# Performance work log

Measured on AMD Instinct MI355X. Metric: run time of the kernel, lower is better.

## Reference

```python
import jax, jax.numpy as jnp
import numpy as np

B, N, C, H = 8, 1024, 1024, 16
D = C // H
DFF = 4 * C
EPS = 1e-6


def _ln(x):
    mu = jnp.mean(x, axis=-1, keepdims=True)
    var = jnp.mean(jnp.square(x - mu), axis=-1, keepdims=True)
    return (x - mu) / jnp.sqrt(var + EPS)


def _modulate(x, shift, scale):
    return x * (1 + scale) + shift


def setup_inputs() -> dict:
    key = jax.random.key(0)
    ks = jax.random.split(key, 12)
    s = 0.02
    inp = {
        "x": jax.random.normal(ks[0], (B, N, C), jnp.float32),
        "c": jax.random.normal(ks[1], (B, 1, C), jnp.float32),
        "causal_mask": jnp.tril(jnp.ones((N, N), jnp.int32))[None, None],  # [1,1,N,N]
        "qkv_w": jax.random.normal(ks[2], (3 * C, C), jnp.float32) * s,
        "qkv_b": jnp.zeros((3 * C,), jnp.float32),
        "proj_w": jax.random.normal(ks[3], (C, C), jnp.float32) * s,
        "proj_b": jnp.zeros((C,), jnp.float32),
        "fc1_w": jax.random.normal(ks[4], (DFF, C), jnp.float32) * s,
        "fc1_b": jnp.zeros((DFF,), jnp.float32),
        "fc2_w": jax.random.normal(ks[5], (C, DFF), jnp.float32) * s,
        "fc2_b": jnp.zeros((C,), jnp.float32),
        "ada_w": jax.random.normal(ks[6], (6 * C, C), jnp.float32) * s,
        "ada_b": jnp.zeros((6 * C,), jnp.float32),
    }
    return inp


def reference(x, c, causal_mask, qkv_w, qkv_b, proj_w, proj_b,
              fc1_w, fc1_b, fc2_w, fc2_b, ada_w, ada_b):
    # adaLN modulation: SiLU -> Linear(C -> 6C) -> chunk 6
    mod = jax.nn.silu(c) @ ada_w.T + ada_b  # [B,1,6C]
    (shift_msa, scale_msa, gate_msa,
     shift_mlp, scale_mlp, gate_mlp) = jnp.split(mod, 6, axis=-1)

    # --- causal attention ---
    y = _modulate(_ln(x), shift_msa, scale_msa)  # [B,N,C]
    qkv = y @ qkv_w.T + qkv_b                    # [B,N,3C]
    qkv = qkv.reshape(B, N, 3, H, D).transpose(2, 0, 3, 1, 4)  # [3,B,H,N,D]
    q, k, v = qkv[0], qkv[1], qkv[2]
    scale = D ** -0.5
    attn = jnp.einsum('bhnd,bhmd->bhnm', q, k) * scale  # [B,H,N,N]
    attn = jnp.where(causal_mask == 0, -jnp.inf, attn)
    attn = jax.nn.softmax(attn, axis=-1)
    o = jnp.einsum('bhnm,bhmd->bhnd', attn, v)
    o = o.transpose(0, 2, 1, 3).reshape(B, N, C)
    o = o @ proj_w.T + proj_b
    x = x + gate_msa * o

    # --- MLP ---
    z = _modulate(_ln(x), shift_mlp, scale_mlp)
    h = jax.nn.gelu(z @ fc1_w.T + fc1_b, approximate=True)
    m = h @ fc2_w.T + fc2_b
    x = x + gate_mlp * m
    return x
```

## Files before the change

kernel.cpp:

```cpp
#include <hip/hip_runtime.h>
#include <math.h>
#include <stdint.h>
#include <stddef.h>

namespace {

constexpr int kB = 8, kN = 1024, kC = 1024, kH = 16, kD = 64, kDFF = 4096;
constexpr int kM = kB * kN;
constexpr int k6C = 6 * kC;
constexpr float kQKScale = 0.18033688011112042f;
constexpr float kM8 = 8.0f;

typedef _Float16 half8 __attribute__((ext_vector_type(8)));
typedef _Float16 half4v __attribute__((ext_vector_type(4)));
typedef float f32x4 __attribute__((ext_vector_type(4)));
typedef int v4i __attribute__((ext_vector_type(4)));
typedef signed char i8;

__device__ inline void ld_lds16(const void* g, void* l) {
  __builtin_amdgcn_global_load_lds(
      (const __attribute__((address_space(1))) void*)g,
      (__attribute__((address_space(3))) void*)l, 16, 0, 0);
}

__device__ inline int xcd_swizzle(int flat, int nwg) {
  return (flat & 7) * (nwg >> 3) + (flat >> 3);
}

__device__ inline unsigned pack4_i8(float y0, float y1, float y2, float y3, float inv) {
  int q0 = (int)rintf(y0 * inv), q1 = (int)rintf(y1 * inv);
  int q2 = (int)rintf(y2 * inv), q3 = (int)rintf(y3 * inv);
  q0 = min(max(q0, -127), 127); q1 = min(max(q1, -127), 127);
  q2 = min(max(q2, -127), 127); q3 = min(max(q3, -127), 127);
  return (unsigned)(q0 & 0xFF) | ((unsigned)(q1 & 0xFF) << 8) |
         ((unsigned)(q2 & 0xFF) << 16) | ((unsigned)(q3 & 0xFF) << 24);
}

__global__ void cvt_f32_f16(const float* __restrict__ src, _Float16* __restrict__ dst) {
  size_t i = (size_t)blockIdx.x * 256 + threadIdx.x;
  float4 f = ((const float4*)src)[i];
  half4v h;
  h[0] = (_Float16)f.x; h[1] = (_Float16)f.y; h[2] = (_Float16)f.z; h[3] = (_Float16)f.w;
  ((half4v*)dst)[i] = h;
}

__global__ __launch_bounds__(256) void quant_w_kernel(
    const float* __restrict__ src, i8* __restrict__ dst, float* __restrict__ wscale) {
  int n = blockIdx.x, tid = threadIdx.x;
  const float* row = src + (size_t)n * kC;
  float4 f = ((const float4*)row)[tid];
  float m = fmaxf(fmaxf(fabsf(f.x), fabsf(f.y)), fmaxf(fabsf(f.z), fabsf(f.w)));
#pragma unroll
  for (int msk = 32; msk; msk >>= 1) m = fmaxf(m, __shfl_xor(m, msk));
  __shared__ float red[4];
  int w = tid >> 6, lane = tid & 63;
  if (lane == 0) red[w] = m;
  __syncthreads();
  m = fmaxf(fmaxf(red[0], red[1]), fmaxf(red[2], red[3]));
  m = fmaxf(m, 1e-12f);
  float inv = 127.f / m;
  ((unsigned*)(dst + (size_t)n * kC))[tid] = pack4_i8(f.x, f.y, f.z, f.w, inv);
  if (tid == 0) wscale[n] = m * (1.f / 127.f);
}

__global__ __launch_bounds__(256) void mod_kernel(
    const float* __restrict__ c, const float* __restrict__ ada_w,
    const float* __restrict__ ada_b, float* __restrict__ mod) {
  __shared__ float sc[kC];
  int b  = blockIdx.x / (k6C / 4);
  int j0 = (blockIdx.x % (k6C / 4)) * 4;
  int tid = threadIdx.x;
  for (int i = tid; i < kC; i += 256) {
    float v = c[b * kC + i];
    sc[i] = v / (1.f + expf(-v));
  }
  __syncthreads();
  int w = tid >> 6, lane = tid & 63;
  int j = j0 + w;
  const float* wr = ada_w + (size_t)j * kC;
  float acc = 0.f;
#pragma unroll
  for (int kk = 0; kk < kC / 64; ++kk) {
    int k = kk * 64 + lane;
    acc += sc[k] * wr[k];
  }
#pragma unroll
  for (int m = 32; m; m >>= 1) acc += __shfl_xor(acc, m);
  if (lane == 0) mod[b * k6C + j] = acc + ada_b[j];
}

template <typename T>
__global__ __launch_bounds__(256) void ln_mod_q_kernel(
    const T* __restrict__ x, const float* __restrict__ mod,
    i8* __restrict__ out, float* __restrict__ ascale,
    int shift_off, int scale_off) {
  int row = blockIdx.x;
  int b = row >> 10;
  const T* xr = x + (size_t)row * kC;
  int tid = threadIdx.x;
  int cc0 = tid * 4;
  float v[4];
  float s = 0.f, s2 = 0.f;
#pragma unroll
  for (int i = 0; i < 4; ++i) {
    v[i] = (float)xr[cc0 + i];
    s += v[i];
    s2 += v[i] * v[i];
  }
#pragma unroll
  for (int m = 32; m; m >>= 1) { s += __shfl_xor(s, m); s2 += __shfl_xor(s2, m); }
  __shared__ float red[8];
  __shared__ float redm[4];
  int w = tid >> 6, lane = tid & 63;
  if (lane == 0) { red[w] = s; red[4 + w] = s2; }
  __syncthreads();
  s  = red[0] + red[1] + red[2] + red[3];
  s2 = red[4] + red[5] + red[6] + red[7];
  float mu   = s * (1.f / kC);
  float var  = s2 * (1.f / kC) - mu * mu;
  float rstd = rsqrtf(var + 1e-6f);
  const float* mb = mod + (size_t)b * k6C;
  float y[4];
  float m = 0.f;
#pragma unroll
  for (int i = 0; i < 4; ++i) {
    y[i] = (v[i] - mu) * rstd * (1.f + mb[scale_off + cc0 + i]) + mb[shift_off + cc0 + i];
    m = fmaxf(m, fabsf(y[i]));
  }
#pragma unroll
  for (int msk = 32; msk; msk >>= 1) m = fmaxf(m, __shfl_xor(m, msk));
  if (lane == 0) redm[w] = m;
  __syncthreads();
  m = fmaxf(fmaxf(redm[0], redm[1]), fmaxf(redm[2], redm[3]));
  m = fmaxf(m, 1e-12f);
  float inv = 127.f / m;
  ((unsigned*)(out + (size_t)row * kC))[tid] = pack4_i8(y[0], y[1], y[2], y[3], inv);
  if (tid == 0) ascale[row] = m * (1.f / 127.f);
}

template <int EPI>
__global__ __launch_bounds__(256, 4) void gemm_i8_kernel(
    const i8* __restrict__ A, const i8* __restrict__ W,
    const float* __restrict__ ascale, const float* __restrict__ wscale,
    const float* __restrict__ bias, _Float16* __restrict__ outp,
    int M, int Nn, int K) {
  __shared__ __align__(16) i8 S[2 * 2 * 128 * 64];
  int tid = threadIdx.x;
  int nwg = (int)(gridDim.x * gridDim.y);
  int swz = xcd_swizzle((int)(blockIdx.y * gridDim.x + blockIdx.x), nwg);
  int bn = swz % (int)gridDim.x, bm = swz / (int)gridDim.x;
  int lane = tid & 63, w = tid >> 6;
  int l15 = lane & 15, quad = lane >> 4;
  int wr = (w >> 1) * 64, wc = (w & 1) * 64;

  v4i acc[4][4];
#pragma unroll
  for (int i = 0; i < 4; ++i)
#pragma unroll
    for (int j = 0; j < 4; ++j) acc[i][j] = (v4i){0, 0, 0, 0};

  const i8* Ag = A + (size_t)bm * 128 * K;
  const i8* Wg = W + (size_t)bn * 128 * K;
  int rg = lane >> 2;
  int gsl = lane & 3;

  auto stage = [&](int buf, int kt) {
    i8* As = S + buf * (2 * 128 * 64);
    i8* Bs = As + 128 * 64;
#pragma unroll
    for (int s = 0; s < 2; ++s) {
      int row = w * 32 + s * 16 + rg;
      int gc = (gsl ^ ((row >> 1) & 3)) * 16;
      ld_lds16(&Ag[(size_t)row * K + kt + gc], &As[(w * 32 + s * 16) * 64]);
      ld_lds16(&Wg[(size_t)row * K + kt + gc], &Bs[(w * 32 + s * 16) * 64]);
    }
  };

  int nk = K >> 6;
  stage(0, 0);
  stage(1, 64);

  int cread = (quad ^ ((l15 >> 1) & 3)) * 16;
  for (int t = 0; t < nk; ++t) {
    if (t + 1 < nk) {
      asm volatile("s_waitcnt vmcnt(4)" ::: "memory");
    } else {
      asm volatile("s_waitcnt vmcnt(0)" ::: "memory");
    }
    __builtin_amdgcn_s_barrier();
    __builtin_amdgcn_sched_barrier(0);
    const i8* As = S + (t & 1) * (2 * 128 * 64);
    const i8* Bs = As + 128 * 64;
    v4i af[4], bf[4];
#pragma unroll
    for (int i = 0; i < 4; ++i)
      af[i] = *(const v4i*)&As[(wr + i * 16 + l15) * 64 + cread];
#pragma unroll
    for (int j = 0; j < 4; ++j)
      bf[j] = *(const v4i*)&Bs[(wc + j * 16 + l15) * 64 + cread];
#pragma unroll
    for (int i = 0; i < 4; ++i)
#pragma unroll
      for (int j = 0; j < 4; ++j)
        acc[i][j] = __builtin_amdgcn_mfma_i32_16x16x64_i8(af[i], bf[j], acc[i][j], 0, 0, 0);
    asm volatile("s_waitcnt lgkmcnt(0)" ::: "memory");
    __builtin_amdgcn_sched_barrier(0);
    __builtin_amdgcn_s_barrier();
    __builtin_amdgcn_sched_barrier(0);
    if (t + 2 < nk) stage(t & 1, (t + 2) << 6);
  }

  _Float16* Cs = (_Float16*)S;
  int row0 = wr + quad * 4;
  int col0 = wc + l15;
#pragma unroll
  for (int i = 0; i < 4; ++i) {
#pragma unroll
    for (int j = 0; j < 4; ++j) {
      int colL = col0 + j * 16;
      int n = bn * 128 + colL;
      float ws = wscale[n];
      float bv = bias[n];
#pragma unroll
      for (int r = 0; r < 4; ++r) {
        int rowL = row0 + i * 16 + r;
        float as = ascale[bm * 128 + rowL];
        float v = (float)acc[i][j][r] * (as * ws) + bv;
        if constexpr (EPI == 0) {
          if (n < kC) v *= kQKScale;
        } else {
          float u = v + 0.044715f * v * v * v;
          float t = exp2f(-2.302208f * u);
          v = v * __builtin_amdgcn_rcpf(1.f + t);
        }
        Cs[rowL * 128 + (((colL >> 3) ^ (rowL & 7)) << 3) + (colL & 7)] = (_Float16)v;
      }
    }
  }
  __syncthreads();
#pragma unroll
  for (int p = 0; p < 8; ++p) {
    int r = (tid >> 4) + p * 16;
    int cc = tid & 15;
    half8 hv = *(const half8*)&Cs[r * 128 + ((cc ^ (r & 7)) << 3)];
    size_t gm = (size_t)(bm * 128 + r);
    int coff = bn * 128 + cc * 8;
    *(half8*)&outp[gm * Nn + coff] = hv;
  }
}

template <int EPI>
__global__ __launch_bounds__(256) void gemm_f16_kernel(
    const _Float16* __restrict__ A, const _Float16* __restrict__ W,
    const float* __restrict__ bias, void* __restrict__ outp,
    const void* __restrict__ resid, const float* __restrict__ mod,
    int M, int Nn, int K, int gate_off) {
  __shared__ __align__(16) _Float16 S[2 * 2 * 128 * 64];
  int tid = threadIdx.x;
  int nwg = (int)(gridDim.x * gridDim.y);
  int swz = xcd_swizzle((int)(blockIdx.y * gridDim.x + blockIdx.x), nwg);
  int bn = swz % (int)gridDim.x, bm = swz / (int)gridDim.x;
  int lane = tid & 63, w = tid >> 6;
  int l15 = lane & 15, quad = lane >> 4;
  int wr = (w >> 1) * 64, wc = (w & 1) * 64;

  f32x4 acc[4][4];
#pragma unroll
  for (int i = 0; i < 4; ++i)
#pragma unroll
    for (int j = 0; j < 4; ++j) acc[i][j] = (f32x4){0.f, 0.f, 0.f, 0.f};

  const _Float16* Ag = A + (size_t)bm * 128 * K;
  const _Float16* Wg = W + (size_t)bn * 128 * K;
  int r8 = lane >> 3;
  int jc = ((lane & 7) ^ r8) * 8;

  auto stage = [&](int buf, int kt) {
    _Float16* Asn = S + buf * (2 * 128 * 64);
    _Float16* Bsn = Asn + 128 * 64;
#pragma unroll
    for (int u = 0; u < 4; ++u) {
      int row = w * 32 + u * 8 + r8;
      ld_lds16(&Ag[(size_t)row * K + kt + jc], &Asn[(w * 32 + u * 8) * 64]);
      ld_lds16(&Wg[(size_t)row * K + kt + jc], &Bsn[(w * 32 + u * 8) * 64]);
    }
  };

  int nk = K / 64;
  stage(0, 0);
  stage(1, 64);

  for (int t = 0; t < nk; ++t) {
    if (t + 1 < nk) {
      asm volatile("s_waitcnt vmcnt(8)" ::: "memory");
    } else {
      asm volatile("s_waitcnt vmcnt(0)" ::: "memory");
    }
    __builtin_amdgcn_s_barrier();
    __builtin_amdgcn_sched_barrier(0);
    const _Float16* As = S + (t & 1) * (2 * 128 * 64);
    const _Float16* Bs = As + 128 * 64;
    half8 af[2][4], bf[2][4];
#pragma unroll
    for (int kk = 0; kk < 2; ++kk) {
#pragma unroll
      for (int i = 0; i < 4; ++i)
        af[kk][i] = *(const half8*)&As[(wr + i * 16 + l15) * 64 +
                                       (((kk * 4 + quad) ^ (l15 & 7)) * 8)];
#pragma unroll
      for (int j = 0; j < 4; ++j)
        bf[kk][j] = *(const half8*)&Bs[(wc + j * 16 + l15) * 64 +
                                       (((kk * 4 + quad) ^ (l15 & 7)) * 8)];
    }
#pragma unroll
    for (int kk = 0; kk < 2; ++kk)
#pragma unroll
      for (int i = 0; i < 4; ++i)
#pragma unroll
        for (int j = 0; j < 4; ++j)
          acc[i][j] = __builtin_amdgcn_mfma_f32_16x16x32_f16(af[kk][i], bf[kk][j],
                                                             acc[i][j], 0, 0, 0);
    asm volatile("s_waitcnt lgkmcnt(0)" ::: "memory");
    __builtin_amdgcn_sched_barrier(0);
    __builtin_amdgcn_s_barrier();
    __builtin_amdgcn_sched_barrier(0);
    if (t + 2 < nk) stage(t & 1, (t + 2) * 64);
  }

  _Float16* Cs = S;
  int row0 = wr + quad * 4;
  int col0 = wc + l15;
#pragma unroll
  for (int i = 0; i < 4; ++i) {
#pragma unroll
    for (int j = 0; j < 4; ++j) {
      int colL = col0 + j * 16;
      int n = bn * 128 + colL;
      float bv = bias[n];
#pragma unroll
      for (int r = 0; r < 4; ++r) {
        int rowL = row0 + i * 16 + r;
        float v = acc[i][j][r] + bv;
        Cs[rowL * 128 + (((colL >> 3) ^ (rowL & 7)) << 3) + (colL & 7)] = (_Float16)v;
      }
    }
  }
  __syncthreads();
  int b6 = (bm >> 3) * k6C + gate_off + bn * 128;
#pragma unroll
  for (int p = 0; p < 8; ++p) {
    int r = (tid >> 4) + p * 16;
    int cc = tid & 15;
    half8 hv = *(const half8*)&Cs[r * 128 + ((cc ^ (r & 7)) << 3)];
    size_t gm = (size_t)(bm * 128 + r);
    int coff = bn * 128 + cc * 8;
    if constexpr (EPI == 2) {
      const float* rp = &((const float*)resid)[gm * kC + coff];
      const float* gp = &mod[b6 + cc * 8];
      half8 ov;
#pragma unroll
      for (int e = 0; e < 8; ++e) ov[e] = (_Float16)(rp[e] + gp[e] * (float)hv[e]);
      *(half8*)&((_Float16*)outp)[gm * kC + coff] = ov;
    } else {
      const _Float16* rp = &((const _Float16*)resid)[gm * kC + coff];
      const float* gp = &mod[b6 + cc * 8];
      half8 rv = *(const half8*)rp;
      float ov[8];
#pragma unroll
      for (int e = 0; e < 8; ++e) ov[e] = (float)rv[e] + gp[e] * (float)hv[e];
      *(float4*)&((float*)outp)[gm * kC + coff] = *(float4*)&ov[0];
      *(float4*)&((float*)outp)[gm * kC + coff + 4] = *(float4*)&ov[4];
    }
  }
}

__global__ __launch_bounds__(256) void vtrans_kernel(
    const _Float16* __restrict__ qkv, _Float16* __restrict__ vT) {
  int nt = blockIdx.x, h = blockIdx.y, b = blockIdx.z;
  __shared__ _Float16 Ts[64 * 72];
  int tid = threadIdx.x;
  const _Float16* src = qkv + ((size_t)(b * kN + nt * 64)) * (3 * kC) + 2 * kC + h * 64;
#pragma unroll
  for (int u = 0; u < 2; ++u) {
    int idx = tid + u * 256;
    int r = idx >> 3, c8 = (idx & 7) * 8;
    *(uint4*)&Ts[r * 72 + c8] = *(const uint4*)&src[(size_t)r * (3 * kC) + c8];
  }
  __syncthreads();
  _Float16* dst = vT + (((size_t)(b * kH + h)) * 64) * kN + nt * 64;
#pragma unroll
  for (int u = 0; u < 2; ++u) {
    int idx = tid + u * 256;
    int d = idx >> 3, n8 = (idx & 7) * 8;
    half8 v;
#pragma unroll
    for (int e = 0; e < 8; ++e) v[e] = Ts[(n8 + e) * 72 + d];
    *(half8*)&dst[(size_t)d * kN + n8] = v;
  }
}

__global__ __launch_bounds__(256, 3) void attn_kernel(
    const _Float16* __restrict__ qkv, const _Float16* __restrict__ vT,
    _Float16* __restrict__ o) {
  int nwg = (int)(gridDim.x * gridDim.y * gridDim.z);
  int flat = (int)((blockIdx.z * gridDim.y + blockIdx.y) * gridDim.x + blockIdx.x);
  int swz = xcd_swizzle(flat, nwg);
  int qt = swz % (int)gridDim.x;
  int tmp = swz / (int)gridDim.x;
  int h = tmp % (int)gridDim.y, b = tmp / (int)gridDim.y;
  __shared__ __align__(16) _Float16 S[2 * 8192 + 128 * 72];
  _Float16* Ps = S + 16384;
  int tid = threadIdx.x, lane = tid & 63, w = tid >> 6;
  int l15 = lane & 15, quad = lane >> 4;
  int wq = w * 32;
  int r8 = lane >> 3;
  int jc = ((lane & 7) ^ r8) * 8;

  const _Float16* Qg = qkv + ((size_t)(b * kN + qt * 128)) * (3 * kC) + h * kD;
  const _Float16* Kg = qkv + ((size_t)(b * kN)) * (3 * kC) + kC + h * kD;
  const _Float16* Vg = vT + ((size_t)(b * kH + h) * kD) * kN;

  auto stage_kv = [&](_Float16* dstK, int j) {
#pragma unroll
    for (int u = 0; u < 2; ++u) {
      int row = w * 16 + u * 8 + r8;
      ld_lds16(&Kg[(size_t)(j * 64 + row) * (3 * kC) + jc], &dstK[(w * 16 + u * 8) * 64]);
      ld_lds16(&Vg[(size_t)row * kN + j * 64 + jc], &dstK[4096 + (w * 16 + u * 8) * 64]);
    }
  };

#pragma unroll
  for (int u = 0; u < 4; ++u)
    ld_lds16(&Qg[(size_t)(w * 32 + u * 8 + r8) * (3 * kC) + jc],
             &S[(w * 32 + u * 8) * 64]);
  stage_kv(S + 8192, 0);
  asm volatile("s_waitcnt vmcnt(4)" ::: "memory");
  __builtin_amdgcn_s_barrier();

  half8 aq[2][2];
#pragma unroll
  for (int i = 0; i < 2; ++i)
#pragma unroll
    for (int kk = 0; kk < 2; ++kk)
      aq[i][kk] = *(const half8*)&S[(wq + i * 16 + l15) * 64 +
                                    (((kk * 4 + quad) ^ (l15 & 7)) * 8)];
  asm volatile("s_waitcnt lgkmcnt(0)" ::: "memory");
  __builtin_amdgcn_sched_barrier(0);
  __builtin_amdgcn_s_barrier();
  stage_kv(S, 1);

  f32x4 o_acc[2][4];
  f32x4 lsum[2];
#pragma unroll
  for (int i = 0; i < 2; ++i) {
    lsum[i] = (f32x4){0.f, 0.f, 0.f, 0.f};
#pragma unroll
    for (int dt = 0; dt < 4; ++dt) o_acc[i][dt] = (f32x4){0.f, 0.f, 0.f, 0.f};
  }
  half8 ones;
#pragma unroll
  for (int e = 0; e < 8; ++e) ones[e] = (_Float16)1.f;

  int jmax = 2 * qt + 2;
  for (int j = 0; j < jmax; ++j) {
    if (j + 1 < jmax) {
      asm volatile("s_waitcnt vmcnt(4)" ::: "memory");
    } else {
      asm volatile("s_waitcnt vmcnt(0)" ::: "memory");
    }
    __builtin_amdgcn_s_barrier();
    __builtin_amdgcn_sched_barrier(0);
    const _Float16* Ks = (j & 1) ? S : S + 8192;
    const _Float16* Vs = Ks + 4096;
    bool need_mask = (j >= 2 * qt);

    f32x4 s[2][4];
#pragma unroll
    for (int ct = 0; ct < 4; ++ct) {
      half8 b0 = *(const half8*)&Ks[(ct * 16 + l15) * 64 + ((quad ^ (l15 & 7)) * 8)];
      half8 b1 = *(const half8*)&Ks[(ct * 16 + l15) * 64 + (((4 + quad) ^ (l15 & 7)) * 8)];
#pragma unroll
      for (int i = 0; i < 2; ++i) {
        f32x4 t = (f32x4){0.f, 0.f, 0.f, 0.f};
        t = __builtin_amdgcn_mfma_f32_16x16x32_f16(aq[i][0], b0, t, 0, 0, 0);
        t = __builtin_amdgcn_mfma_f32_16x16x32_f16(aq[i][1], b1, t, 0, 0, 0);
        s[i][ct] = t;
      }
    }

#pragma unroll
    for (int i = 0; i < 2; ++i)
#pragma unroll
      for (int ct = 0; ct < 4; ++ct)
#pragma unroll
        for (int r = 0; r < 4; ++r) {
          float p = exp2f(fminf(s[i][ct][r] - kM8, 14.f));
          if (need_mask) {
            int kg = j * 64 + ct * 16 + l15;
            int qg = qt * 128 + wq + i * 16 + quad * 4 + r;
            if (kg > qg) p = 0.f;
          }
          Ps[(wq + i * 16 + quad * 4 + r) * 72 + ct * 16 + l15] = (_Float16)p;
        }

    half8 bv0[4], bv1[4];
#pragma unroll
    for (int dt = 0; dt < 4; ++dt) {
      bv0[dt] = *(const half8*)&Vs[(dt * 16 + l15) * 64 + ((quad ^ (l15 & 7)) * 8)];
      bv1[dt] = *(const half8*)&Vs[(dt * 16 + l15) * 64 + (((4 + quad) ^ (l15 & 7)) * 8)];
    }
    asm volatile("s_waitcnt lgkmcnt(0)" ::: "memory");
    __builtin_amdgcn_sched_barrier(0);
    __builtin_amdgcn_s_barrier();
    __builtin_amdgcn_sched_barrier(0);
    if (j + 2 < jmax)
      stage_kv((j & 1) ? S : S + 8192, j + 2);

    half8 ap[2][2];
#pragma unroll
    for (int i = 0; i < 2; ++i) {
      ap[i][0] = *(const half8*)&Ps[(wq + i * 16 + l15) * 72 + quad * 8];
      ap[i][1] = *(const half8*)&Ps[(wq + i * 16 + l15) * 72 + 32 + quad * 8];
      lsum[i] = __builtin_amdgcn_mfma_f32_16x16x32_f16(ap[i][0], ones, lsum[i], 0, 0, 0);
      lsum[i] = __builtin_amdgcn_mfma_f32_16x16x32_f16(ap[i][1], ones, lsum[i], 0, 0, 0);
    }
#pragma unroll
    for (int dt = 0; dt < 4; ++dt)
#pragma unroll
      for (int i = 0; i < 2; ++i) {
        o_acc[i][dt] = __builtin_amdgcn_mfma_f32_16x16x32_f16(ap[i][0], bv0[dt], o_acc[i][dt], 0, 0, 0);
        o_acc[i][dt] = __builtin_amdgcn_mfma_f32_16x16x32_f16(ap[i][1], bv1[dt], o_acc[i][dt], 0, 0, 0);
      }
  }

#pragma unroll
  for (int i = 0; i < 2; ++i) {
    float rl[4];
#pragma unroll
    for (int r = 0; r < 4; ++r) rl[r] = __builtin_amdgcn_rcpf(lsum[i][r]);
#pragma unroll
    for (int dt = 0; dt < 4; ++dt)
#pragma unroll
      for (int r = 0; r < 4; ++r) {
        int q = qt * 128 + wq + i * 16 + quad * 4 + r;
        o[((size_t)(b * kN + q)) * kC + h * kD + dt * 16 + l15] =
            (_Float16)(o_acc[i][dt][r] * rl[r]);
      }
  }
}

}

extern "C" void kernel_launch(void* const* d_in, const int* in_sizes, int n_in,
                              void* d_out, int out_size, void* d_ws, size_t ws_size,
                              hipStream_t stream) {
  const float* x      = (const float*)d_in[0];
  const float* c      = (const float*)d_in[1];
  const float* qkv_w  = (const float*)d_in[3];
  const float* qkv_b  = (const float*)d_in[4];
  const float* proj_w = (const float*)d_in[5];
  const float* proj_b = (const float*)d_in[6];
  const float* fc1_w  = (const float*)d_in[7];
  const float* fc1_b  = (const float*)d_in[8];
  const float* fc2_w  = (const float*)d_in[9];
  const float* fc2_b  = (const float*)d_in[10];
  const float* ada_w  = (const float*)d_in[11];
  const float* ada_b  = (const float*)d_in[12];
  float* out = (float*)d_out;

  char* ws = (char*)d_ws;
  float*    mod     = (float*)(ws);
  i8*       w_qkv   = (i8*)(ws + 196608);
  i8*       w_fc1   = (i8*)(ws + 3342336);
  _Float16* w_proj  = (_Float16*)(ws + 7536640);
  _Float16* w_fc2   = (_Float16*)(ws + 9633792);
  i8*       bufA    = (i8*)(ws + 18022400);
  float*    ascale  = (float*)(ws + 26411008);
  float*    ws_qkv  = (float*)(ws + 26443776);
  float*    ws_fc1  = (float*)(ws + 26456064);
  _Float16* vT      = (_Float16*)(ws + 26509312);
  _Float16* x2h     = (_Float16*)(ws + 26509312);
  _Float16* bufO    = (_Float16*)(ws + 43286528);
  _Float16* qkvh    = (_Float16*)(ws + 60063744);
  _Float16* hbuf    = (_Float16*)(ws + 60063744);

  quant_w_kernel<<<3 * kC, 256, 0, stream>>>(qkv_w, w_qkv, ws_qkv);
  quant_w_kernel<<<kDFF, 256, 0, stream>>>(fc1_w, w_fc1, ws_fc1);
  cvt_f32_f16<<<kC * kC / 1024, 256, 0, stream>>>(proj_w, w_proj);
  cvt_f32_f16<<<kC * kDFF / 1024, 256, 0, stream>>>(fc2_w, w_fc2);
  mod_kernel<<<kB * (k6C / 4), 256, 0, stream>>>(c, ada_w, ada_b, mod);
  ln_mod_q_kernel<float><<<kM, 256, 0, stream>>>(x, mod, bufA, ascale, 0, kC);
  gemm_i8_kernel<0><<<dim3(3 * kC / 128, kM / 128), 256, 0, stream>>>(
      bufA, w_qkv, ascale, ws_qkv, qkv_b, qkvh, kM, 3 * kC, kC);
  vtrans_kernel<<<dim3(kN / 64, kH, kB), 256, 0, stream>>>(qkvh, vT);
  attn_kernel<<<dim3(kN / 128, kH, kB), 256, 0, stream>>>(qkvh, vT, bufO);
  gemm_f16_kernel<2><<<dim3(kC / 128, kM / 128), 256, 0, stream>>>(
      bufO, w_proj, proj_b, x2h, x, mod, kM, kC, kC, 2 * kC);
  ln_mod_q_kernel<_Float16><<<kM, 256, 0, stream>>>(x2h, mod, bufA, ascale, 3 * kC, 4 * kC);
  gemm_i8_kernel<1><<<dim3(kDFF / 128, kM / 128), 256, 0, stream>>>(
      bufA, w_fc1, ascale, ws_fc1, fc1_b, hbuf, kM, kDFF, kC);
  gemm_f16_kernel<3><<<dim3(kC / 128, kM / 128), 256, 0, stream>>>(
      hbuf, w_fc2, fc2_b, out, x2h, mod, kM, kC, kDFF, 5 * kC);
}
```

Baseline: 469.9 us.

## Load f16 GEMM weights straight to registers and overlap staging with MFMA

In the f16 GEMM, the weight (B) tile is no longer staged through LDS. Each wave loads its B fragments from global memory directly into a register double-buffer (even and odd halves), while only A stays double-buffered in LDS. The K loop is unrolled by two, with vmcnt waits re-counted to match the new loads. In the int8 GEMM, the barrier and next-stage prefetch now happen before the MFMAs instead of after, so global loads overlap the math. The goals are to halve LDS traffic and LDS footprint and to hide load latency. The risks are uncoalesced global B loads, duplicated B reads across waves, and higher register pressure.

```diff
diff --git a/kernel.cpp b/kernel.cpp
--- a/kernel.cpp
+++ b/kernel.cpp
@@ -198,16 +198,16 @@
 #pragma unroll
     for (int j = 0; j < 4; ++j)
       bf[j] = *(const v4i*)&Bs[(wc + j * 16 + l15) * 64 + cread];
+    asm volatile("s_waitcnt lgkmcnt(0)" ::: "memory");
+    __builtin_amdgcn_sched_barrier(0);
+    __builtin_amdgcn_s_barrier();
+    __builtin_amdgcn_sched_barrier(0);
+    if (t + 2 < nk) stage(t & 1, (t + 2) << 6);
 #pragma unroll
     for (int i = 0; i < 4; ++i)
 #pragma unroll
       for (int j = 0; j < 4; ++j)
         acc[i][j] = __builtin_amdgcn_mfma_i32_16x16x64_i8(af[i], bf[j], acc[i][j], 0, 0, 0);
-    asm volatile("s_waitcnt lgkmcnt(0)" ::: "memory");
-    __builtin_amdgcn_sched_barrier(0);
-    __builtin_amdgcn_s_barrier();
-    __builtin_amdgcn_sched_barrier(0);
-    if (t + 2 < nk) stage(t & 1, (t + 2) << 6);
   }
 
   _Float16* Cs = (_Float16*)S;
@@ -255,7 +255,7 @@
     const float* __restrict__ bias, void* __restrict__ outp,
     const void* __restrict__ resid, const float* __restrict__ mod,
     int M, int Nn, int K, int gate_off) {
-  __shared__ __align__(16) _Float16 S[2 * 2 * 128 * 64];
+  __shared__ __align__(16) _Float16 S[2 * 128 * 64];
   int tid = threadIdx.x;
   int nwg = (int)(gridDim.x * gridDim.y);
   int swz = xcd_swizzle((int)(blockIdx.y * gridDim.x + blockIdx.x), nwg);
@@ -275,56 +275,92 @@
   int r8 = lane >> 3;
   int jc = ((lane & 7) ^ r8) * 8;
 
-  auto stage = [&](int buf, int kt) {
-    _Float16* Asn = S + buf * (2 * 128 * 64);
-    _Float16* Bsn = Asn + 128 * 64;
+  auto stageA = [&](int buf, int kt) {
+    _Float16* As = S + buf * (128 * 64);
 #pragma unroll
     for (int u = 0; u < 4; ++u) {
       int row = w * 32 + u * 8 + r8;
-      ld_lds16(&Ag[(size_t)row * K + kt + jc], &Asn[(w * 32 + u * 8) * 64]);
-      ld_lds16(&Wg[(size_t)row * K + kt + jc], &Bsn[(w * 32 + u * 8) * 64]);
+      ld_lds16(&Ag[(size_t)row * K + kt + jc], &As[(w * 32 + u * 8) * 64]);
     }
   };
+  auto loadB = [&](half8 (&bf)[2][4], int kt) {
+#pragma unroll
+    for (int kk = 0; kk < 2; ++kk)
+#pragma unroll
+      for (int j = 0; j < 4; ++j)
+        bf[kk][j] = *(const half8*)&Wg[(size_t)(wc + j * 16 + l15) * K + kt +
+                                       (kk * 4 + quad) * 8];
+  };
 
   int nk = K / 64;
-  stage(0, 0);
-  stage(1, 64);
-
-  for (int t = 0; t < nk; ++t) {
+  half8 bfE[2][4], bfO[2][4];
+  stageA(0, 0);
+  loadB(bfE, 0);
+  stageA(1, 64);
+
+  for (int t = 0; t < nk; t += 2) {
     if (t + 1 < nk) {
-      asm volatile("s_waitcnt vmcnt(8)" ::: "memory");
+      asm volatile("s_waitcnt vmcnt(4)" ::: "memory");
     } else {
       asm volatile("s_waitcnt vmcnt(0)" ::: "memory");
     }
     __builtin_amdgcn_s_barrier();
     __builtin_amdgcn_sched_barrier(0);
-    const _Float16* As = S + (t & 1) * (2 * 128 * 64);
-    const _Float16* Bs = As + 128 * 64;
-    half8 af[2][4], bf[2][4];
-#pragma unroll
-    for (int kk = 0; kk < 2; ++kk) {
-#pragma unroll
-      for (int i = 0; i < 4; ++i)
-        af[kk][i] = *(const half8*)&As[(wr + i * 16 + l15) * 64 +
-                                       (((kk * 4 + quad) ^ (l15 & 7)) * 8)];
-#pragma unroll
-      for (int j = 0; j < 4; ++j)
-        bf[kk][j] = *(const half8*)&Bs[(wc + j * 16 + l15) * 64 +
-                                       (((kk * 4 + quad) ^ (l15 & 7)) * 8)];
-    }
-#pragma unroll
-    for (int kk = 0; kk < 2; ++kk)
-#pragma unroll
-      for (int i = 0; i < 4; ++i)
-#pragma unroll
-        for (int j = 0; j < 4; ++j)
-          acc[i][j] = __builtin_amdgcn_mfma_f32_16x16x32_f16(af[kk][i], bf[kk][j],
-                                                             acc[i][j], 0, 0, 0);
-    asm volatile("s_waitcnt lgkmcnt(0)" ::: "memory");
-    __builtin_amdgcn_sched_barrier(0);
+    {
+      const _Float16* As = S;
+      half8 af[2][4];
+#pragma unroll
+      for (int kk = 0; kk < 2; ++kk)
+#pragma unroll
+        for (int i = 0; i < 4; ++i)
+          af[kk][i] = *(const half8*)&As[(wr + i * 16 + l15) * 64 +
+                                         (((kk * 4 + quad) ^ (l15 & 7)) * 8)];
+      asm volatile("s_waitcnt lgkmcnt(0)" ::: "memory");
+      __builtin_amdgcn_sched_barrier(0);
+      __builtin_amdgcn_s_barrier();
+      __builtin_amdgcn_sched_barrier(0);
+      if (t + 1 < nk) loadB(bfO, (t + 1) * 64);
+      if (t + 2 < nk) stageA(0, (t + 2) * 64);
+#pragma unroll
+      for (int kk = 0; kk < 2; ++kk)
+#pragma unroll
+        for (int i = 0; i < 4; ++i)
+#pragma unroll
+          for (int j = 0; j < 4; ++j)
+            acc[i][j] = __builtin_amdgcn_mfma_f32_16x16x32_f16(af[kk][i], bfE[kk][j],
+                                                               acc[i][j], 0, 0, 0);
+    }
+    if (t + 2 < nk) {
+      asm volatile("s_waitcnt vmcnt(4)" ::: "memory");
+    } else {
+      asm volatile("s_waitcnt vmcnt(0)" ::: "memory");
+    }
     __builtin_amdgcn_s_barrier();
     __builtin_amdgcn_sched_barrier(0);
-    if (t + 2 < nk) stage(t & 1, (t + 2) * 64);
+    {
+      const _Float16* As = S + 128 * 64;
+      half8 af[2][4];
+#pragma unroll
+      for (int kk = 0; kk < 2; ++kk)
+#pragma unroll
+        for (int i = 0; i < 4; ++i)
+          af[kk][i] = *(const half8*)&As[(wr + i * 16 + l15) * 64 +
+                                         (((kk * 4 + quad) ^ (l15 & 7)) * 8)];
+      asm volatile("s_waitcnt lgkmcnt(0)" ::: "memory");
+      __builtin_amdgcn_sched_barrier(0);
+      __builtin_amdgcn_s_barrier();
+      __builtin_amdgcn_sched_barrier(0);
+      if (t + 2 < nk) loadB(bfE, (t + 2) * 64);
+      if (t + 3 < nk) stageA(1, (t + 3) * 64);
+#pragma unroll
+      for (int kk = 0; kk < 2; ++kk)
+#pragma unroll
+        for (int i = 0; i < 4; ++i)
+#pragma unroll
+          for (int j = 0; j < 4; ++j)
+            acc[i][j] = __builtin_amdgcn_mfma_f32_16x16x32_f16(af[kk][i], bfO[kk][j],
+                                                               acc[i][j], 0, 0, 0);
+    }
   }
 
   _Float16* Cs = S;
```

After: 558.3 us. 1.19x slower.
